# Kernel tuning notes

Measured on AMD Instinct MI355X. Metric: run time of the kernel, lower is better.

Reference implementation:

```python
import jax, jax.numpy as jnp
import numpy as np

NUM_WIRES = 14
N_LAYERS = 4
BATCH = 128


def _rx_mat(theta):
    # PennyLane RX(t) = [[cos(t/2), -i sin(t/2)], [-i sin(t/2), cos(t/2)]]
    c = jnp.cos(theta / 2).astype(jnp.complex64)
    s = jnp.sin(theta / 2).astype(jnp.complex64)
    row0 = jnp.stack([c, -1j * s], axis=-1)
    row1 = jnp.stack([-1j * s, c], axis=-1)
    return jnp.stack([row0, row1], axis=-2)  # (..., 2, 2)


def _rz_mat(theta):
    # PennyLane RZ(t) = diag(exp(-it/2), exp(it/2))
    e0 = jnp.exp(-1j * theta.astype(jnp.complex64) / 2)
    e1 = jnp.exp(1j * theta.astype(jnp.complex64) / 2)
    z = jnp.zeros_like(e0)
    row0 = jnp.stack([e0, z], axis=-1)
    row1 = jnp.stack([z, e1], axis=-1)
    return jnp.stack([row0, row1], axis=-2)


def _apply_1q(psi, gate, wire):
    # psi: (B, 2, 2, ..., 2); gate: (2,2) shared or (B,2,2) per-sample
    axis = wire + 1
    psi = jnp.moveaxis(psi, axis, -1)
    if gate.ndim == 2:
        psi = psi @ gate.T
    else:
        psi = jnp.einsum('b...j,bij->b...i', psi, gate)
    return jnp.moveaxis(psi, -1, axis)


def _apply_cnot(psi, ctrl, tgt):
    ac, at = ctrl + 1, tgt + 1
    psi0 = jnp.take(psi, 0, axis=ac)
    psi1 = jnp.take(psi, 1, axis=ac)
    at_adj = at - (1 if at > ac else 0)  # target axis shifts after removing ctrl axis
    psi1 = jnp.flip(psi1, axis=at_adj)   # X on target when ctrl=1
    return jnp.stack([psi0, psi1], axis=ac)


def _circuit(x, weights):
    # x: (B, n) real angles; weights: (L, n, 2)
    B = x.shape[0]
    n = NUM_WIRES
    psi = jnp.zeros((B,) + (2,) * n, jnp.complex64)
    psi = psi.at[(slice(None),) + (0,) * n].set(1.0)  # |0...0>
    # data encoding: per-sample RX gates
    for i in range(n):
        psi = _apply_1q(psi, _rx_mat(x[:, i]), i)
    # variational ansatz
    for l in range(N_LAYERS):
        for i in range(n):
            psi = _apply_1q(psi, _rx_mat(weights[l, i, 0]), i)
            psi = _apply_1q(psi, _rz_mat(weights[l, i, 1]), i)
        for i in range(n - 1):
            psi = _apply_cnot(psi, i, i + 1)
        psi = _apply_cnot(psi, n - 1, 0)
    # <Z_i> for every wire
    p = jnp.abs(psi) ** 2  # (B, 2, ..., 2) real
    zs = []
    for i in range(n):
        other = tuple(a for a in range(1, n + 1) if a != i + 1)
        m = jnp.sum(p, axis=other)  # (B, 2)
        zs.append(m[:, 0] - m[:, 1])
    return jnp.stack(zs, axis=-1)  # (B, n)


def setup_inputs() -> dict:
    key = jax.random.key(0)
    k1, k2, k3, k4 = jax.random.split(key, 4)
    states = jax.random.normal(k1, (BATCH, 2 ** NUM_WIRES), dtype=jnp.float32)
    weights = jax.random.normal(k2, (N_LAYERS, NUM_WIRES, 2), dtype=jnp.float32)
    lim = 1.0 / np.sqrt(NUM_WIRES)
    head_w = jax.random.uniform(k3, (1, NUM_WIRES), jnp.float32, -lim, lim)
    head_b = jax.random.uniform(k4, (1,), jnp.float32, -lim, lim)
    return {"states": states, "weights": weights, "head_w": head_w, "head_b": head_b}


def reference(states, weights, head_w, head_b):
    features = jnp.abs(states)[:, :NUM_WIRES]        # (B, n)
    qfeatures = _circuit(features, weights)          # (B, n)
    out = (qfeatures @ head_w.T + head_b)[:, 0]      # (B,)
    return out
```

## Files before the change

kernel.cpp:

```cpp
#include <hip/hip_runtime.h>
#include <math.h>

#define NW 14
#define NSTATE 16384
#define HALF 8192
#define NL 4
#define BATCH 128
#define TPB 1024
#define SHBYTES (84 * 1024)


__device__ __forceinline__ unsigned sxmap(unsigned v) {
    unsigned t = v;
    t ^= t >> 1; t ^= t >> 2; t ^= t >> 4; t ^= t >> 8;
    return (t & 0x0FFFu) | ((t & 1u) << 13);
}

__device__ __forceinline__ float2 cmul(float2 u, float2 v) {
    return make_float2(u.x * v.x - u.y * v.y, u.x * v.y + u.y * v.x);
}

__device__ __forceinline__ float4 fused_coef(const float* weights,
                                             const float* states,
                                             int b, int l, int w) {
    float t1 = weights[(l * NW + w) * 2 + 0];
    float t2 = weights[(l * NW + w) * 2 + 1];
    if (l == 0) t1 += fabsf(states[(size_t)b * NSTATE + w]);
    float s, c, sz, cz;
    sincosf(0.5f * t1, &s, &c);
    sincosf(0.5f * t2, &sz, &cz);
    return make_float4(c * cz, -c * sz, -s * sz, -s * cz);
}

template<int N, int M>
__device__ __forceinline__ void gateN(float2* r, float4 g, unsigned s3) {
    const float f = (s3 & (unsigned)M) ? -1.0f : 1.0f;
    g.y *= f;
    g.z *= f;
#pragma unroll
    for (int k = 0; k < N; ++k) {
        if ((k & M) == 0) {
            const float x0 = r[k].x,   y0 = r[k].y;
            const float x1 = r[k|M].x, y1 = r[k|M].y;
            r[k].x   =  g.x*x0 - g.y*y0 + g.z*x1 - g.w*y1;
            r[k].y   =  g.x*y0 + g.y*x0 + g.z*y1 + g.w*x1;
            r[k|M].x = -g.z*x0 - g.w*y0 + g.x*x1 + g.y*y1;
            r[k|M].y = -g.z*y0 + g.w*x0 + g.x*y1 - g.y*x1;
        }
    }
}

template<int J0, int S3SH, int S3MSK>
__device__ __forceinline__ void pass3(float2* psi, const float4* gc,
                                      unsigned t) {
    const float4 gA = gc[13 - (J0 + 0)];
    const float4 gB = gc[13 - (J0 + 1)];
    const float4 gC = gc[13 - (J0 + 2)];
    const unsigned s3   = (t >> S3SH) & (unsigned)S3MSK;
    const unsigned low  = t & ((1u << J0) - 1u);
    const unsigned high = (t >> J0) << (J0 + 3);
    float2 r[8];
#pragma unroll
    for (int k = 0; k < 8; ++k)
        r[k] = psi[low | (((unsigned)k ^ s3) << J0) | high];
    gateN<8,1>(r, gA, s3);
    gateN<8,2>(r, gB, s3);
    gateN<8,4>(r, gC, s3);
#pragma unroll
    for (int k = 0; k < 8; ++k)
        psi[low | (((unsigned)k ^ s3) << J0) | high] = r[k];
}

__device__ __forceinline__ void exit_scatter(const float2* psi,
                                             float2* __restrict__ dst,
                                             float4 g1, unsigned q,
                                             unsigned tid) {
#pragma unroll
    for (int m = 0; m < 4; ++m) {
        const unsigned jc = tid + (unsigned)m * TPB;
        const float2 x0 = psi[jc];
        const float2 x1 = psi[jc | 0x1000u];
        float2 A0, A1;
        A0.x =  g1.x*x0.x - g1.y*x0.y + g1.z*x1.x - g1.w*x1.y;
        A0.y =  g1.x*x0.y + g1.y*x0.x + g1.z*x1.y + g1.w*x1.x;
        A1.x = -g1.z*x0.x - g1.w*x0.y + g1.x*x1.x + g1.y*x1.y;
        A1.y = -g1.z*x0.y + g1.w*x0.x + g1.x*x1.y - g1.y*x1.x;
        const unsigned d0 = sxmap(jc) ^ (q ? 0x1FFFu : 0u);
        dst[d0]           = A0;
        dst[d0 ^ 0x3FFFu] = A1;
    }
}

__global__ __launch_bounds__(TPB) void k_layer1(
    const float* __restrict__ states, const float* __restrict__ weights,
    float2* __restrict__ Sout)
{
    extern __shared__ float2 psi[];
    __shared__ float2 vfac[NW][2];
    __shared__ float2 T1[128];
    __shared__ float2 T2[128];
    __shared__ float4 gc[NW];
    const unsigned gid = blockIdx.x, q = gid >> 7, b = gid & 127u;
    const unsigned tid = threadIdx.x;

    if (tid < NW) {
        float4 g = fused_coef(weights, states, (int)b, 0, (int)tid);
        vfac[tid][0] = make_float2(g.x, g.y);
        vfac[tid][1] = make_float2(-g.z, g.w);
    }
    if (tid >= 64 && tid < 64 + NW)
        gc[tid - 64] = fused_coef(weights, states, (int)b, 1, (int)(tid - 64));
    __syncthreads();
    if (tid < 128) {
        float2 p = make_float2(1.0f, 0.0f);
#pragma unroll
        for (int j = 0; j < 7; ++j)
            p = cmul(p, vfac[13 - j][(tid >> j) & 1u]);
        T1[tid] = p;
    } else if (tid < 256) {
        const unsigned u = tid - 128;
        float2 p = make_float2(1.0f, 0.0f);
#pragma unroll
        for (int j = 7; j < 14; ++j)
            p = cmul(p, vfac[13 - j][(u >> (j - 7)) & 1u]);
        T2[u] = p;
    }
    __syncthreads();

#pragma unroll
    for (int m = 0; m < 8; ++m) {
        const unsigned I  = tid + (unsigned)m * TPB;
        const unsigned If = I | (q << 13);
        const unsigned lo = (If ^ (If >> 1)) & 0x0FFFu;
        const unsigned y12 = ((If >> 12) ^ (If >> 13) ^ If) & 1u;
        const unsigned y13 = ((If >> 13) ^ If) & 1u;
        const unsigned J = lo | (y12 << 12) | (y13 << 13);
        psi[I] = cmul(T1[J & 127u], T2[J >> 7]);
    }
    __syncthreads();

    pass3<0, 1, 7>(psi, gc, tid);  __syncthreads();
    pass3<3, 3, 1>(psi, gc, tid);  __syncthreads();
    pass3<6, 0, 0>(psi, gc, tid);  __syncthreads();
    pass3<9, 0, 0>(psi, gc, tid);  __syncthreads();

    exit_scatter(psi, Sout + (size_t)b * NSTATE, gc[1], q, tid);
}

template<int L>
__global__ __launch_bounds__(TPB) void k_layer(
    const float* __restrict__ states, const float* __restrict__ weights,
    const float2* __restrict__ Sin, float2* __restrict__ Sout)
{
    extern __shared__ float2 psi[];
    __shared__ float4 gc[NW];
    __shared__ float4 ge_s;
    const unsigned gid = blockIdx.x, q = gid >> 7, b = gid & 127u;
    const unsigned tid = threadIdx.x;

    if (tid < NW) gc[tid] = fused_coef(weights, states, (int)b, L, (int)tid);
    if (tid == NW) ge_s = fused_coef(weights, states, (int)b, L - 1, 0);
    __syncthreads();
    const float4 ge = ge_s;

    const float2* src = Sin + (size_t)b * NSTATE + (size_t)q * HALF;
#pragma unroll
    for (int m = 0; m < 4; ++m) {
        const unsigned ic = tid + (unsigned)m * TPB;
        const float2 f0 = src[ic];
        const float2 f1 = src[ic ^ 0x1FFFu];
        const unsigned rc = (q ^ ic) & 1u;
        const float aar = ge.x, aai = rc ? -ge.y : ge.y;
        const float bbr = rc ? -ge.z : ge.z, bbi = ge.w;
        float2 oc, op;
        oc.x = aar*f0.x - aai*f0.y + bbr*f1.x - bbi*f1.y;
        oc.y = aar*f0.y + aai*f0.x + bbr*f1.y + bbi*f1.x;
        op.x = aar*f1.x + aai*f1.y - (bbr*f0.x + bbi*f0.y);
        op.y = aar*f1.y - aai*f1.x - (bbr*f0.y - bbi*f0.x);
        psi[ic]           = oc;
        psi[ic ^ 0x1FFFu] = op;
    }
    __syncthreads();

    pass3<0, 1, 7>(psi, gc, tid);  __syncthreads();
    pass3<3, 3, 1>(psi, gc, tid);  __syncthreads();
    pass3<6, 0, 0>(psi, gc, tid);  __syncthreads();
    pass3<9, 0, 0>(psi, gc, tid);  __syncthreads();

    exit_scatter(psi, Sout + (size_t)b * NSTATE, gc[1], q, tid);
}

__global__ __launch_bounds__(TPB) void k_final(
    const float* __restrict__ states, const float* __restrict__ weights,
    const float* __restrict__ head_w, const float* __restrict__ head_b,
    const float2* __restrict__ Sin, float* __restrict__ out)
{
    __shared__ float4 ge_s;
    __shared__ float wsum[TPB / 64];
    const unsigned b = blockIdx.x;
    const unsigned tid = threadIdx.x;

    if (tid == 0) ge_s = fused_coef(weights, states, (int)b, NL - 1, 0);
    __syncthreads();
    const float4 ge = ge_s;

    float hw[NW];
#pragma unroll
    for (int i = 0; i < NW; ++i) hw[i] = head_w[i];

    float hwsumv = 0.0f;
#pragma unroll
    for (int i = 0; i < NW; ++i) hwsumv += hw[i];
    float cvt = hwsumv;
#pragma unroll
    for (int p = 0; p < 10; ++p)
        if ((tid >> p) & 1u) cvt -= 2.0f * hw[13 - p];

    float acc = 0.0f;
#pragma unroll
    for (int qm = 0; qm < 8; ++qm) {
        const unsigned q = (unsigned)qm >> 2;
        const unsigned m = (unsigned)qm & 3u;
        const float2* src = Sin + (size_t)b * NSTATE + (size_t)q * HALF;
        const unsigned ic = tid + m * TPB;
        const float2 f0 = src[ic];
        const float2 f1 = src[ic ^ 0x1FFFu];
        const unsigned rc = (q ^ ic) & 1u;
        const float aar = ge.x, aai = rc ? -ge.y : ge.y;
        const float bbr = rc ? -ge.z : ge.z, bbi = ge.w;
        float2 oc, op;
        oc.x = aar*f0.x - aai*f0.y + bbr*f1.x - bbi*f1.y;
        oc.y = aar*f0.y + aai*f0.x + bbr*f1.y + bbi*f1.x;
        op.x = aar*f1.x + aai*f1.y - (bbr*f0.x + bbi*f0.y);
        op.y = aar*f1.y - aai*f1.x - (bbr*f0.y - bbi*f0.x);
        float cv_c = cvt;
        if (q) cv_c -= 2.0f * hw[0];
        if (m & 1) cv_c -= 2.0f * hw[3];
        if (m & 2) cv_c -= 2.0f * hw[2];
        const float s0w = 1.0f - 2.0f * (float)q;
        const float cv_p = 2.0f * hw[0] * s0w - cv_c;
        acc += (oc.x*oc.x + oc.y*oc.y) * cv_c
             + (op.x*op.x + op.y*op.y) * cv_p;
    }
#pragma unroll
    for (int off = 32; off > 0; off >>= 1)
        acc += __shfl_down(acc, off, 64);
    if ((tid & 63u) == 0) wsum[tid >> 6] = acc;
    __syncthreads();
    if (tid == 0) {
        float tot = 0.0f;
#pragma unroll
        for (int i = 0; i < TPB / 64; ++i) tot += wsum[i];
        out[b] = tot + head_b[0];
    }
}

extern "C" void kernel_launch(void* const* d_in, const int* in_sizes, int n_in,
                              void* d_out, int out_size, void* d_ws, size_t ws_size,
                              hipStream_t stream) {
    const float* states  = (const float*)d_in[0];
    const float* weights = (const float*)d_in[1];
    const float* head_w  = (const float*)d_in[2];
    const float* head_b  = (const float*)d_in[3];
    float* out = (float*)d_out;

    float2* SA = (float2*)d_ws;
    float2* SB = SA + (size_t)BATCH * NSTATE;

    k_layer1  <<<2 * BATCH, TPB, SHBYTES, stream>>>(states, weights, SA);
    k_layer<2><<<2 * BATCH, TPB, SHBYTES, stream>>>(states, weights, SA, SB);
    k_layer<3><<<2 * BATCH, TPB, SHBYTES, stream>>>(states, weights, SB, SA);
    k_final   <<<BATCH, TPB, 0, stream>>>(states, weights, head_w, head_b,
                                          SA, out);
}
```

Measured before the change: 114.7 us.

## Fuse layer kernels into one cooperative kernel with pairwise half-state exchange

Replaces the four separate layer kernels with a single cooperative kernel. Each block keeps its half of the state vector in shared memory across all layers and exchanges only the partner-owned half through small global inboxes, with grid.sync between layers. This is meant to remove kernel launch gaps and the full state round trips through global memory. In exchange it depends on all 256 blocks being co-resident for the cooperative launch, pays the cost of grid-wide barriers, and needs a memset plus atomicAdd to combine the two per-sample partial outputs.

```diff
diff --git a/kernel.cpp b/kernel.cpp
--- a/kernel.cpp
+++ b/kernel.cpp
@@ -1,13 +1,17 @@
 #include <hip/hip_runtime.h>
+#include <hip/hip_cooperative_groups.h>
 #include <math.h>
+
+namespace cg = cooperative_groups;
 
 #define NW 14
 #define NSTATE 16384
 #define HALF 8192
+#define QHALF 4096
 #define NL 4
 #define BATCH 128
 #define TPB 1024
-#define SHBYTES (84 * 1024)
+#define SHBYTES (2 * HALF * (int)sizeof(float2))
 
 
 __device__ __forceinline__ unsigned sxmap(unsigned v) {
@@ -18,6 +22,18 @@
 
 __device__ __forceinline__ float2 cmul(float2 u, float2 v) {
     return make_float2(u.x * v.x - u.y * v.y, u.x * v.y + u.y * v.x);
+}
+
+__device__ __forceinline__ void ag_store(float2* p, float2 v) {
+    __hip_atomic_store(reinterpret_cast<unsigned long long*>(p),
+                       __builtin_bit_cast(unsigned long long, v),
+                       __ATOMIC_RELAXED, __HIP_MEMORY_SCOPE_AGENT);
+}
+__device__ __forceinline__ float2 ag_load(const float2* p) {
+    unsigned long long u = __hip_atomic_load(
+        reinterpret_cast<const unsigned long long*>(p),
+        __ATOMIC_RELAXED, __HIP_MEMORY_SCOPE_AGENT);
+    return __builtin_bit_cast(float2, u);
 }
 
 __device__ __forceinline__ float4 fused_coef(const float* weights,
@@ -71,45 +87,85 @@
         psi[low | (((unsigned)k ^ s3) << J0) | high] = r[k];
 }
 
-__device__ __forceinline__ void exit_scatter(const float2* psi,
-                                             float2* __restrict__ dst,
-                                             float4 g1, unsigned q,
-                                             unsigned tid) {
+__device__ __forceinline__ void exit_exchange(const float2* psiA,
+                                              float2* psiB, float2* inboxP,
+                                              float4 g1, unsigned q,
+                                              unsigned tid) {
 #pragma unroll
     for (int m = 0; m < 4; ++m) {
         const unsigned jc = tid + (unsigned)m * TPB;
-        const float2 x0 = psi[jc];
-        const float2 x1 = psi[jc | 0x1000u];
+        const float2 x0 = psiA[jc];
+        const float2 x1 = psiA[jc | 0x1000u];
         float2 A0, A1;
         A0.x =  g1.x*x0.x - g1.y*x0.y + g1.z*x1.x - g1.w*x1.y;
         A0.y =  g1.x*x0.y + g1.y*x0.x + g1.z*x1.y + g1.w*x1.x;
         A1.x = -g1.z*x0.x - g1.w*x0.y + g1.x*x1.x + g1.y*x1.y;
         A1.y = -g1.z*x0.y + g1.w*x0.x + g1.x*x1.y - g1.y*x1.x;
         const unsigned d0 = sxmap(jc) ^ (q ? 0x1FFFu : 0u);
-        dst[d0]           = A0;
-        dst[d0 ^ 0x3FFFu] = A1;
-    }
-}
-
-__global__ __launch_bounds__(TPB) void k_layer1(
+        const unsigned d1 = d0 ^ 0x3FFFu;
+        const bool loc0 = (d0 >> 13) == q;
+        const float2  La = loc0 ? A0 : A1;
+        const unsigned Ls = (loc0 ? d0 : d1) & 0x1FFFu;
+        const float2  Ra = loc0 ? A1 : A0;
+        const unsigned Rs = ((loc0 ? d1 : d0) & 0x1FFFu) >> 1;
+        psiB[Ls] = La;
+        ag_store(inboxP + Rs, Ra);
+    }
+}
+
+__device__ __forceinline__ void merge_entry(const float2* psiB,
+                                            const float2* inbox,
+                                            float2* psiA, float4 ge,
+                                            unsigned q, unsigned tid) {
+    const float aar = ge.x, aai = q ? -ge.y : ge.y;
+    const float bbr = q ? -ge.z : ge.z, bbi = ge.w;
+#pragma unroll
+    for (int m = 0; m < 4; ++m) {
+        const unsigned se = 2u * (tid + (unsigned)m * TPB);
+        const unsigned so = se ^ 0x1FFFu;
+        const float2 f0 = psiB[se];
+        const float2 f1 = ag_load(inbox + (so >> 1));
+        float2 oc, op;
+        oc.x = aar*f0.x - aai*f0.y + bbr*f1.x - bbi*f1.y;
+        oc.y = aar*f0.y + aai*f0.x + bbr*f1.y + bbi*f1.x;
+        op.x = aar*f1.x + aai*f1.y - (bbr*f0.x + bbi*f0.y);
+        op.y = aar*f1.y - aai*f1.x - (bbr*f0.y - bbi*f0.x);
+        psiA[se] = oc;
+        psiA[so] = op;
+    }
+}
+
+__global__ __launch_bounds__(TPB) void qsim_coop(
     const float* __restrict__ states, const float* __restrict__ weights,
-    float2* __restrict__ Sout)
+    const float* __restrict__ head_w, const float* __restrict__ head_b,
+    float2* __restrict__ EX0, float2* __restrict__ EX1,
+    float* __restrict__ out)
 {
-    extern __shared__ float2 psi[];
+    extern __shared__ float2 dyn[];
+    float2* psiA = dyn;
+    float2* psiB = dyn + HALF;
+    __shared__ float4 gc4[NL * NW];
     __shared__ float2 vfac[NW][2];
     __shared__ float2 T1[128];
     __shared__ float2 T2[128];
-    __shared__ float4 gc[NW];
+    __shared__ float wsum[TPB / 64];
+
+    cg::grid_group grid = cg::this_grid();
     const unsigned gid = blockIdx.x, q = gid >> 7, b = gid & 127u;
     const unsigned tid = threadIdx.x;
-
+    float2* inboxMine0 = EX0 + (size_t)gid * QHALF;
+    float2* inboxPart0 = EX0 + (size_t)(gid ^ 128u) * QHALF;
+    float2* inboxMine1 = EX1 + (size_t)gid * QHALF;
+    float2* inboxPart1 = EX1 + (size_t)(gid ^ 128u) * QHALF;
+
+    if (tid < NL * NW)
+        gc4[tid] = fused_coef(weights, states, (int)b,
+                              (int)tid / NW, (int)tid % NW);
+    __syncthreads();
     if (tid < NW) {
-        float4 g = fused_coef(weights, states, (int)b, 0, (int)tid);
-        vfac[tid][0] = make_float2(g.x, g.y);
-        vfac[tid][1] = make_float2(-g.z, g.w);
-    }
-    if (tid >= 64 && tid < 64 + NW)
-        gc[tid - 64] = fused_coef(weights, states, (int)b, 1, (int)(tid - 64));
+        vfac[tid][0] = make_float2(gc4[tid].x, gc4[tid].y);
+        vfac[tid][1] = make_float2(-gc4[tid].z, gc4[tid].w);
+    }
     __syncthreads();
     if (tid < 128) {
         float2 p = make_float2(1.0f, 0.0f);
@@ -131,113 +187,73 @@
     for (int m = 0; m < 8; ++m) {
         const unsigned I  = tid + (unsigned)m * TPB;
         const unsigned If = I | (q << 13);
-        const unsigned lo = (If ^ (If >> 1)) & 0x0FFFu;
+        const unsigned lo  = (If ^ (If >> 1)) & 0x0FFFu;
         const unsigned y12 = ((If >> 12) ^ (If >> 13) ^ If) & 1u;
         const unsigned y13 = ((If >> 13) ^ If) & 1u;
         const unsigned J = lo | (y12 << 12) | (y13 << 13);
-        psi[I] = cmul(T1[J & 127u], T2[J >> 7]);
-    }
-    __syncthreads();
-
-    pass3<0, 1, 7>(psi, gc, tid);  __syncthreads();
-    pass3<3, 3, 1>(psi, gc, tid);  __syncthreads();
-    pass3<6, 0, 0>(psi, gc, tid);  __syncthreads();
-    pass3<9, 0, 0>(psi, gc, tid);  __syncthreads();
-
-    exit_scatter(psi, Sout + (size_t)b * NSTATE, gc[1], q, tid);
-}
-
-template<int L>
-__global__ __launch_bounds__(TPB) void k_layer(
-    const float* __restrict__ states, const float* __restrict__ weights,
-    const float2* __restrict__ Sin, float2* __restrict__ Sout)
-{
-    extern __shared__ float2 psi[];
-    __shared__ float4 gc[NW];
-    __shared__ float4 ge_s;
-    const unsigned gid = blockIdx.x, q = gid >> 7, b = gid & 127u;
-    const unsigned tid = threadIdx.x;
-
-    if (tid < NW) gc[tid] = fused_coef(weights, states, (int)b, L, (int)tid);
-    if (tid == NW) ge_s = fused_coef(weights, states, (int)b, L - 1, 0);
-    __syncthreads();
-    const float4 ge = ge_s;
-
-    const float2* src = Sin + (size_t)b * NSTATE + (size_t)q * HALF;
+        psiA[I] = cmul(T1[J & 127u], T2[J >> 7]);
+    }
+    __syncthreads();
+
+    pass3<0, 1, 7>(psiA, gc4 + 1 * NW, tid);  __syncthreads();
+    pass3<3, 3, 1>(psiA, gc4 + 1 * NW, tid);  __syncthreads();
+    pass3<6, 0, 0>(psiA, gc4 + 1 * NW, tid);  __syncthreads();
+    pass3<9, 0, 0>(psiA, gc4 + 1 * NW, tid);  __syncthreads();
+    exit_exchange(psiA, psiB, inboxPart0, gc4[1 * NW + 1], q, tid);
+    __threadfence();
+    grid.sync();
+    merge_entry(psiB, inboxMine0, psiA, gc4[1 * NW + 0], q, tid);
+    __syncthreads();
+
+    pass3<0, 1, 7>(psiA, gc4 + 2 * NW, tid);  __syncthreads();
+    pass3<3, 3, 1>(psiA, gc4 + 2 * NW, tid);  __syncthreads();
+    pass3<6, 0, 0>(psiA, gc4 + 2 * NW, tid);  __syncthreads();
+    pass3<9, 0, 0>(psiA, gc4 + 2 * NW, tid);  __syncthreads();
+    exit_exchange(psiA, psiB, inboxPart1, gc4[2 * NW + 1], q, tid);
+    __threadfence();
+    grid.sync();
+    merge_entry(psiB, inboxMine1, psiA, gc4[2 * NW + 0], q, tid);
+    __syncthreads();
+
+    pass3<0, 1, 7>(psiA, gc4 + 3 * NW, tid);  __syncthreads();
+    pass3<3, 3, 1>(psiA, gc4 + 3 * NW, tid);  __syncthreads();
+    pass3<6, 0, 0>(psiA, gc4 + 3 * NW, tid);  __syncthreads();
+    pass3<9, 0, 0>(psiA, gc4 + 3 * NW, tid);  __syncthreads();
+    exit_exchange(psiA, psiB, inboxPart0, gc4[3 * NW + 1], q, tid);
+    __threadfence();
+    grid.sync();
+
+    const float4 ge = gc4[3 * NW + 0];
+    const float aar = ge.x, aai = q ? -ge.y : ge.y;
+    const float bbr = q ? -ge.z : ge.z, bbi = ge.w;
+
+    float hw[NW];
+#pragma unroll
+    for (int i = 0; i < NW; ++i) hw[i] = head_w[i];
+    float cvt = 0.0f;
+#pragma unroll
+    for (int i = 0; i < NW; ++i) cvt += hw[i];
+    if (q) cvt -= 2.0f * hw[0];
+#pragma unroll
+    for (int p = 0; p < 10; ++p)
+        if ((tid >> p) & 1u) cvt -= 2.0f * hw[12 - p];
+    const float s0w = 1.0f - 2.0f * (float)q;
+
+    float acc = 0.0f;
 #pragma unroll
     for (int m = 0; m < 4; ++m) {
-        const unsigned ic = tid + (unsigned)m * TPB;
-        const float2 f0 = src[ic];
-        const float2 f1 = src[ic ^ 0x1FFFu];
-        const unsigned rc = (q ^ ic) & 1u;
-        const float aar = ge.x, aai = rc ? -ge.y : ge.y;
-        const float bbr = rc ? -ge.z : ge.z, bbi = ge.w;
-        float2 oc, op;
-        oc.x = aar*f0.x - aai*f0.y + bbr*f1.x - bbi*f1.y;
-        oc.y = aar*f0.y + aai*f0.x + bbr*f1.y + bbi*f1.x;
-        op.x = aar*f1.x + aai*f1.y - (bbr*f0.x + bbi*f0.y);
-        op.y = aar*f1.y - aai*f1.x - (bbr*f0.y - bbi*f0.x);
-        psi[ic]           = oc;
-        psi[ic ^ 0x1FFFu] = op;
-    }
-    __syncthreads();
-
-    pass3<0, 1, 7>(psi, gc, tid);  __syncthreads();
-    pass3<3, 3, 1>(psi, gc, tid);  __syncthreads();
-    pass3<6, 0, 0>(psi, gc, tid);  __syncthreads();
-    pass3<9, 0, 0>(psi, gc, tid);  __syncthreads();
-
-    exit_scatter(psi, Sout + (size_t)b * NSTATE, gc[1], q, tid);
-}
-
-__global__ __launch_bounds__(TPB) void k_final(
-    const float* __restrict__ states, const float* __restrict__ weights,
-    const float* __restrict__ head_w, const float* __restrict__ head_b,
-    const float2* __restrict__ Sin, float* __restrict__ out)
-{
-    __shared__ float4 ge_s;
-    __shared__ float wsum[TPB / 64];
-    const unsigned b = blockIdx.x;
-    const unsigned tid = threadIdx.x;
-
-    if (tid == 0) ge_s = fused_coef(weights, states, (int)b, NL - 1, 0);
-    __syncthreads();
-    const float4 ge = ge_s;
-
-    float hw[NW];
-#pragma unroll
-    for (int i = 0; i < NW; ++i) hw[i] = head_w[i];
-
-    float hwsumv = 0.0f;
-#pragma unroll
-    for (int i = 0; i < NW; ++i) hwsumv += hw[i];
-    float cvt = hwsumv;
-#pragma unroll
-    for (int p = 0; p < 10; ++p)
-        if ((tid >> p) & 1u) cvt -= 2.0f * hw[13 - p];
-
-    float acc = 0.0f;
-#pragma unroll
-    for (int qm = 0; qm < 8; ++qm) {
-        const unsigned q = (unsigned)qm >> 2;
-        const unsigned m = (unsigned)qm & 3u;
-        const float2* src = Sin + (size_t)b * NSTATE + (size_t)q * HALF;
-        const unsigned ic = tid + m * TPB;
-        const float2 f0 = src[ic];
-        const float2 f1 = src[ic ^ 0x1FFFu];
-        const unsigned rc = (q ^ ic) & 1u;
-        const float aar = ge.x, aai = rc ? -ge.y : ge.y;
-        const float bbr = rc ? -ge.z : ge.z, bbi = ge.w;
+        const unsigned se = 2u * (tid + (unsigned)m * TPB);
+        const unsigned so = se ^ 0x1FFFu;
+        const float2 f0 = psiB[se];
+        const float2 f1 = ag_load(inboxMine0 + (so >> 1));
         float2 oc, op;
         oc.x = aar*f0.x - aai*f0.y + bbr*f1.x - bbi*f1.y;
         oc.y = aar*f0.y + aai*f0.x + bbr*f1.y + bbi*f1.x;
         op.x = aar*f1.x + aai*f1.y - (bbr*f0.x + bbi*f0.y);
         op.y = aar*f1.y - aai*f1.x - (bbr*f0.y - bbi*f0.x);
         float cv_c = cvt;
-        if (q) cv_c -= 2.0f * hw[0];
-        if (m & 1) cv_c -= 2.0f * hw[3];
-        if (m & 2) cv_c -= 2.0f * hw[2];
-        const float s0w = 1.0f - 2.0f * (float)q;
+        if (m & 1) cv_c -= 2.0f * hw[2];
+        if (m & 2) cv_c -= 2.0f * hw[1];
         const float cv_p = 2.0f * hw[0] * s0w - cv_c;
         acc += (oc.x*oc.x + oc.y*oc.y) * cv_c
              + (op.x*op.x + op.y*op.y) * cv_p;
@@ -251,7 +267,8 @@
         float tot = 0.0f;
 #pragma unroll
         for (int i = 0; i < TPB / 64; ++i) tot += wsum[i];
-        out[b] = tot + head_b[0];
+        if (q == 0) tot += head_b[0];
+        atomicAdd(out + b, tot);
     }
 }
 
@@ -264,12 +281,12 @@
     const float* head_b  = (const float*)d_in[3];
     float* out = (float*)d_out;
 
-    float2* SA = (float2*)d_ws;
-    float2* SB = SA + (size_t)BATCH * NSTATE;
-
-    k_layer1  <<<2 * BATCH, TPB, SHBYTES, stream>>>(states, weights, SA);
-    k_layer<2><<<2 * BATCH, TPB, SHBYTES, stream>>>(states, weights, SA, SB);
-    k_layer<3><<<2 * BATCH, TPB, SHBYTES, stream>>>(states, weights, SB, SA);
-    k_final   <<<BATCH, TPB, 0, stream>>>(states, weights, head_w, head_b,
-                                          SA, out);
-}
+    float2* EX0 = (float2*)d_ws;
+    float2* EX1 = EX0 + (size_t)256 * QHALF;
+
+    hipMemsetAsync(out, 0, BATCH * sizeof(float), stream);
+    void* args[] = {(void*)&states, (void*)&weights, (void*)&head_w,
+                    (void*)&head_b, (void*)&EX0, (void*)&EX1, (void*)&out};
+    hipLaunchCooperativeKernel((const void*)qsim_coop, dim3(2 * BATCH),
+                               dim3(TPB), args, (unsigned)SHBYTES, stream);
+}
```

After: 398.8 us. +247.8%, slower.

## Fuse layers 2-4 and final measurement into one shared-memory-resident kernel

Applied to the files above, without the earlier changes.

Replaces the two per-layer kernels and the final reduction kernel with a single kernel per batch sample that keeps the full 16384-amplitude state in shared memory. The in-shared passE applies the CNOT-ring permutation and the wire-0/1 gates, and the last layer's expectation is evaluated directly from shared memory. This removes two global state round-trips and two launches, but halves the grid to 128 blocks with about 152KB of shared memory each, so parallelism and occupancy drop.

```diff
diff --git a/kernel.cpp b/kernel.cpp
--- a/kernel.cpp
+++ b/kernel.cpp
@@ -7,8 +7,14 @@
 #define NL 4
 #define BATCH 128
 #define TPB 1024
-#define SHBYTES (84 * 1024)
-
+#define SHB1 (84 * 1024)
+#define SHB2 ((NSTATE + 3 * TPB) * (int)sizeof(float2))
+
+
+#define B4_  0x201Fu
+#define B5_  0x203Fu
+#define B12_ 0x3FFFu
+#define B13_ 0x1FFFu
 
 __device__ __forceinline__ unsigned sxmap(unsigned v) {
     unsigned t = v;
@@ -51,8 +57,8 @@
 }
 
 template<int J0, int S3SH, int S3MSK>
-__device__ __forceinline__ void pass3(float2* psi, const float4* gc,
-                                      unsigned t) {
+__device__ __forceinline__ void pass3h(float2* psi, const float4* gc,
+                                       unsigned t) {
     const float4 gA = gc[13 - (J0 + 0)];
     const float4 gB = gc[13 - (J0 + 1)];
     const float4 gC = gc[13 - (J0 + 2)];
@@ -69,6 +75,82 @@
 #pragma unroll
     for (int k = 0; k < 8; ++k)
         psi[low | (((unsigned)k ^ s3) << J0) | high] = r[k];
+}
+
+template<int J0, int S3SH, int S3MSK>
+__device__ __forceinline__ void pass3f(float2* psi, const float4* gc,
+                                       unsigned t) {
+    const float4 gA = gc[13 - (J0 + 0)];
+    const float4 gB = gc[13 - (J0 + 1)];
+    const float4 gC = gc[13 - (J0 + 2)];
+    const unsigned s3 = (t >> S3SH) & (unsigned)S3MSK;
+#pragma unroll
+    for (int m = 0; m < 2; ++m) {
+        const unsigned x    = t | ((unsigned)m << 10);
+        const unsigned low  = x & ((1u << J0) - 1u);
+        const unsigned high = (x >> J0) << (J0 + 3);
+        float2 r[8];
+#pragma unroll
+        for (int k = 0; k < 8; ++k)
+            r[k] = psi[low | (((unsigned)k ^ s3) << J0) | high];
+        gateN<8,1>(r, gA, s3);
+        gateN<8,2>(r, gB, s3);
+        gateN<8,4>(r, gC, s3);
+#pragma unroll
+        for (int k = 0; k < 8; ++k)
+            psi[low | (((unsigned)k ^ s3) << J0) | high] = r[k];
+    }
+}
+
+__device__ __forceinline__ void passE(float2* psi, float2* spare,
+                                      const float4* gc4, int l, unsigned t) {
+    const float4 g1 = gc4[l*NW + 1];
+    const float4 g0 = gc4[l*NW + 0];
+
+    unsigned v = t;
+    v ^= v >> 1; v ^= v >> 2; v ^= v >> 4; v ^= v >> 8;
+    const unsigned Rinv0 = (v & 0x0FFFu) | ((v & 1u) << 13);
+
+    float2 c0[4];
+#pragma unroll
+    for (int k = 0; k < 4; ++k) c0[k] = psi[t | ((unsigned)k << 12)];
+    gateN<4,1>(c0, g1, 0u);
+    gateN<4,2>(c0, g0, 0u);
+    spare[3*t+0] = c0[1];
+    spare[3*t+1] = c0[2];
+    spare[3*t+2] = c0[3];
+    const float2 keep = c0[0];
+
+    float2 r[12];
+#pragma unroll
+    for (int m = 1; m < 4; ++m) {
+        const unsigned base = t | ((unsigned)m << 10);
+#pragma unroll
+        for (int k = 0; k < 4; ++k)
+            r[(m-1)*4 + k] = psi[base | ((unsigned)k << 12)];
+    }
+#pragma unroll
+    for (int m = 0; m < 3; ++m) {
+        gateN<4,1>(r + 4*m, g1, 0u);
+        gateN<4,2>(r + 4*m, g0, 0u);
+    }
+
+    __syncthreads();
+
+#pragma unroll
+    for (int m = 1; m < 4; ++m) {
+        const unsigned Rb = Rinv0 ^ ((m & 1) ? 0x27FFu : 0u)
+                                  ^ ((m & 2) ? 0x2FFFu : 0u);
+#pragma unroll
+        for (int k = 0; k < 4; ++k) {
+            const unsigned CK = ((k & 1) ? B12_ : 0u) ^ ((k & 2) ? B13_ : 0u);
+            psi[Rb ^ CK] = r[(m-1)*4 + k];
+        }
+    }
+    psi[Rinv0]           = keep;
+    psi[Rinv0 ^ B12_]    = spare[3*t+0];
+    psi[Rinv0 ^ B13_]    = spare[3*t+1];
+    psi[Rinv0 ^ 0x2000u] = spare[3*t+2];
 }
 
 __device__ __forceinline__ void exit_scatter(const float2* psi,
@@ -131,7 +213,7 @@
     for (int m = 0; m < 8; ++m) {
         const unsigned I  = tid + (unsigned)m * TPB;
         const unsigned If = I | (q << 13);
-        const unsigned lo = (If ^ (If >> 1)) & 0x0FFFu;
+        const unsigned lo  = (If ^ (If >> 1)) & 0x0FFFu;
         const unsigned y12 = ((If >> 12) ^ (If >> 13) ^ If) & 1u;
         const unsigned y13 = ((If >> 13) ^ If) & 1u;
         const unsigned J = lo | (y12 << 12) | (y13 << 13);
@@ -139,108 +221,107 @@
     }
     __syncthreads();
 
-    pass3<0, 1, 7>(psi, gc, tid);  __syncthreads();
-    pass3<3, 3, 1>(psi, gc, tid);  __syncthreads();
-    pass3<6, 0, 0>(psi, gc, tid);  __syncthreads();
-    pass3<9, 0, 0>(psi, gc, tid);  __syncthreads();
+    pass3h<0, 1, 7>(psi, gc, tid);  __syncthreads();
+    pass3h<3, 3, 1>(psi, gc, tid);  __syncthreads();
+    pass3h<6, 0, 0>(psi, gc, tid);  __syncthreads();
+    pass3h<9, 0, 0>(psi, gc, tid);  __syncthreads();
 
     exit_scatter(psi, Sout + (size_t)b * NSTATE, gc[1], q, tid);
 }
 
-template<int L>
-__global__ __launch_bounds__(TPB) void k_layer(
-    const float* __restrict__ states, const float* __restrict__ weights,
-    const float2* __restrict__ Sin, float2* __restrict__ Sout)
-{
-    extern __shared__ float2 psi[];
-    __shared__ float4 gc[NW];
-    __shared__ float4 ge_s;
-    const unsigned gid = blockIdx.x, q = gid >> 7, b = gid & 127u;
-    const unsigned tid = threadIdx.x;
-
-    if (tid < NW) gc[tid] = fused_coef(weights, states, (int)b, L, (int)tid);
-    if (tid == NW) ge_s = fused_coef(weights, states, (int)b, L - 1, 0);
-    __syncthreads();
-    const float4 ge = ge_s;
-
-    const float2* src = Sin + (size_t)b * NSTATE + (size_t)q * HALF;
-#pragma unroll
-    for (int m = 0; m < 4; ++m) {
-        const unsigned ic = tid + (unsigned)m * TPB;
-        const float2 f0 = src[ic];
-        const float2 f1 = src[ic ^ 0x1FFFu];
-        const unsigned rc = (q ^ ic) & 1u;
-        const float aar = ge.x, aai = rc ? -ge.y : ge.y;
-        const float bbr = rc ? -ge.z : ge.z, bbi = ge.w;
-        float2 oc, op;
-        oc.x = aar*f0.x - aai*f0.y + bbr*f1.x - bbi*f1.y;
-        oc.y = aar*f0.y + aai*f0.x + bbr*f1.y + bbi*f1.x;
-        op.x = aar*f1.x + aai*f1.y - (bbr*f0.x + bbi*f0.y);
-        op.y = aar*f1.y - aai*f1.x - (bbr*f0.y - bbi*f0.x);
-        psi[ic]           = oc;
-        psi[ic ^ 0x1FFFu] = op;
-    }
-    __syncthreads();
-
-    pass3<0, 1, 7>(psi, gc, tid);  __syncthreads();
-    pass3<3, 3, 1>(psi, gc, tid);  __syncthreads();
-    pass3<6, 0, 0>(psi, gc, tid);  __syncthreads();
-    pass3<9, 0, 0>(psi, gc, tid);  __syncthreads();
-
-    exit_scatter(psi, Sout + (size_t)b * NSTATE, gc[1], q, tid);
-}
-
-__global__ __launch_bounds__(TPB) void k_final(
+__global__ __launch_bounds__(TPB) void k_rest(
     const float* __restrict__ states, const float* __restrict__ weights,
     const float* __restrict__ head_w, const float* __restrict__ head_b,
     const float2* __restrict__ Sin, float* __restrict__ out)
 {
-    __shared__ float4 ge_s;
+    extern __shared__ float2 dyn[];
+    float2* psi   = dyn;
+    float2* spare = dyn + NSTATE;
+    __shared__ float4 gc4[NL * NW];
     __shared__ float wsum[TPB / 64];
     const unsigned b = blockIdx.x;
     const unsigned tid = threadIdx.x;
 
-    if (tid == 0) ge_s = fused_coef(weights, states, (int)b, NL - 1, 0);
-    __syncthreads();
-    const float4 ge = ge_s;
+    if (tid < NL * NW)
+        gc4[tid] = fused_coef(weights, states, (int)b,
+                              (int)tid / NW, (int)tid % NW);
+    __syncthreads();
+
+    {
+        const float4 ge = gc4[1 * NW + 0];
+#pragma unroll
+        for (int qm = 0; qm < 8; ++qm) {
+            const unsigned q = (unsigned)qm >> 2;
+            const unsigned m = (unsigned)qm & 3u;
+            const float2* src = Sin + (size_t)b * NSTATE + (size_t)q * HALF;
+            const unsigned ic = tid + m * TPB;
+            const float2 f0 = src[ic];
+            const float2 f1 = src[ic ^ 0x1FFFu];
+            const unsigned rc = (q ^ ic) & 1u;
+            const float aar = ge.x, aai = rc ? -ge.y : ge.y;
+            const float bbr = rc ? -ge.z : ge.z, bbi = ge.w;
+            float2 oc, op;
+            oc.x = aar*f0.x - aai*f0.y + bbr*f1.x - bbi*f1.y;
+            oc.y = aar*f0.y + aai*f0.x + bbr*f1.y + bbi*f1.x;
+            op.x = aar*f1.x + aai*f1.y - (bbr*f0.x + bbi*f0.y);
+            op.y = aar*f1.y - aai*f1.x - (bbr*f0.y - bbi*f0.x);
+            psi[(q << 13) | ic]            = oc;
+            psi[(q << 13) | (ic ^ 0x1FFFu)] = op;
+        }
+    }
+    __syncthreads();
+
+    pass3f<0, 1, 7>(psi, gc4 + 2 * NW, tid);  __syncthreads();
+    pass3f<3, 3, 1>(psi, gc4 + 2 * NW, tid);  __syncthreads();
+    pass3f<6, 0, 0>(psi, gc4 + 2 * NW, tid);  __syncthreads();
+    pass3f<9, 0, 0>(psi, gc4 + 2 * NW, tid);  __syncthreads();
+    passE(psi, spare, gc4, 2, tid);           __syncthreads();
+
+    pass3f<0, 1, 7>(psi, gc4 + 3 * NW, tid);  __syncthreads();
+    pass3f<3, 3, 1>(psi, gc4 + 3 * NW, tid);  __syncthreads();
+    pass3f<6, 0, 0>(psi, gc4 + 3 * NW, tid);  __syncthreads();
+    pass3f<9, 0, 0>(psi, gc4 + 3 * NW, tid);  __syncthreads();
 
     float hw[NW];
 #pragma unroll
     for (int i = 0; i < NW; ++i) hw[i] = head_w[i];
-
-    float hwsumv = 0.0f;
-#pragma unroll
-    for (int i = 0; i < NW; ++i) hwsumv += hw[i];
-    float cvt = hwsumv;
-#pragma unroll
-    for (int p = 0; p < 10; ++p)
-        if ((tid >> p) & 1u) cvt -= 2.0f * hw[13 - p];
+    float H = 0.0f, H12 = 0.0f;
+#pragma unroll
+    for (int i = 0; i < NW; ++i) H += hw[i];
+#pragma unroll
+    for (int i = 2; i < NW; ++i) H12 += hw[i];
+
+    const float4 g1 = gc4[3 * NW + 1];
+    const float4 g0 = gc4[3 * NW + 0];
 
     float acc = 0.0f;
 #pragma unroll
-    for (int qm = 0; qm < 8; ++qm) {
-        const unsigned q = (unsigned)qm >> 2;
-        const unsigned m = (unsigned)qm & 3u;
-        const float2* src = Sin + (size_t)b * NSTATE + (size_t)q * HALF;
-        const unsigned ic = tid + m * TPB;
-        const float2 f0 = src[ic];
-        const float2 f1 = src[ic ^ 0x1FFFu];
-        const unsigned rc = (q ^ ic) & 1u;
-        const float aar = ge.x, aai = rc ? -ge.y : ge.y;
-        const float bbr = rc ? -ge.z : ge.z, bbi = ge.w;
-        float2 oc, op;
-        oc.x = aar*f0.x - aai*f0.y + bbr*f1.x - bbi*f1.y;
-        oc.y = aar*f0.y + aai*f0.x + bbr*f1.y + bbi*f1.x;
-        op.x = aar*f1.x + aai*f1.y - (bbr*f0.x + bbi*f0.y);
-        op.y = aar*f1.y - aai*f1.x - (bbr*f0.y - bbi*f0.x);
-        float cv_c = cvt;
-        if (q) cv_c -= 2.0f * hw[0];
-        if (m & 1) cv_c -= 2.0f * hw[3];
-        if (m & 2) cv_c -= 2.0f * hw[2];
-        const float s0w = 1.0f - 2.0f * (float)q;
-        const float cv_p = 2.0f * hw[0] * s0w - cv_c;
-        acc += (oc.x*oc.x + oc.y*oc.y) * cv_c
-             + (op.x*op.x + op.y*op.y) * cv_p;
+    for (int m2 = 0; m2 < 4; ++m2) {
+        const unsigned base = tid | ((unsigned)m2 << 10);
+        float2 r[4];
+#pragma unroll
+        for (int k = 0; k < 4; ++k)
+            r[k] = psi[base | ((unsigned)k << 12)];
+        gateN<4,1>(r, g1, 0u);
+        gateN<4,2>(r, g0, 0u);
+        float A = 0.0f;
+        unsigned sfx = 0u;
+#pragma unroll
+        for (int p = 11; p >= 0; --p) {
+            sfx ^= (base >> p) & 1u;
+            if (sfx) A += hw[13 - p];
+        }
+        const unsigned P = sfx;
+#pragma unroll
+        for (int k = 0; k < 4; ++k) {
+            const unsigned u   = ((unsigned)k ^ ((unsigned)k >> 1)) & 1u;
+            const unsigned b13 = P ^ ((unsigned)k & 1u);
+            float sum = u ? (H12 - A) : A;
+            if (u)   sum += hw[1];
+            if (b13) sum += hw[0];
+            const float cv = H - 2.0f * sum;
+            acc += (r[k].x * r[k].x + r[k].y * r[k].y) * cv;
+        }
     }
 #pragma unroll
     for (int off = 32; off > 0; off >>= 1)
@@ -265,11 +346,8 @@
     float* out = (float*)d_out;
 
     float2* SA = (float2*)d_ws;
-    float2* SB = SA + (size_t)BATCH * NSTATE;
-
-    k_layer1  <<<2 * BATCH, TPB, SHBYTES, stream>>>(states, weights, SA);
-    k_layer<2><<<2 * BATCH, TPB, SHBYTES, stream>>>(states, weights, SA, SB);
-    k_layer<3><<<2 * BATCH, TPB, SHBYTES, stream>>>(states, weights, SB, SA);
-    k_final   <<<BATCH, TPB, 0, stream>>>(states, weights, head_w, head_b,
-                                          SA, out);
-}
+
+    k_layer1<<<2 * BATCH, TPB, SHB1, stream>>>(states, weights, SA);
+    k_rest  <<<BATCH, TPB, SHB2, stream>>>(states, weights, head_w, head_b,
+                                           SA, out);
+}
```

After: 102.5 us. 1.12x faster.
